# Kernel optimization log

Measured on AMD Instinct MI355X. Metric: run time of the kernel, lower is better.

The kernel has to match this reference:

```python
import jax, jax.numpy as jnp
import numpy as np

D = 256   # input_size
H = 512   # hidden_size
A = 4     # alpha_dim
K = 2 * A * A  # output values per input dim (binary=False -> 2 params)


def _masks():
    # MADE sequential-ordering masks, per DART.create_masks
    in_deg = np.arange(D)
    hid_deg = np.arange(H) % (D - 1)
    out_deg = np.arange(D) - 1  # arange(D) % D - 1
    m0 = (hid_deg[:, None] >= in_deg[None, :]).astype(np.float32)   # [H, D]
    mh = (hid_deg[:, None] >= hid_deg[None, :]).astype(np.float32)  # [H, H]
    ml = (out_deg[:, None] >= hid_deg[None, :]).astype(np.float32)  # [D, H]
    # repeat(1, K).view(-1, H): each output-dim row repeated K consecutive times
    ml = np.repeat(ml, K, axis=0)                                    # [D*K, H]
    return jnp.asarray(m0), jnp.asarray(mh), jnp.asarray(ml)


def setup_inputs() -> dict:
    key = jax.random.key(0)
    ks = jax.random.split(key, 10)
    B = 1024
    x = jax.random.normal(ks[0], (B, D), dtype=jnp.float32)
    def lin(k, out_dim, in_dim):
        s = 1.0 / np.sqrt(in_dim)
        kw, kb = jax.random.split(k)
        W = jax.random.uniform(kw, (out_dim, in_dim), jnp.float32, -s, s)
        b = jax.random.uniform(kb, (out_dim,), jnp.float32, -s, s)
        return W, b
    W0, b0 = lin(ks[1], H, D)
    W1, b1 = lin(ks[2], H, H)
    W2, b2 = lin(ks[3], H, H)
    Wout, bout = lin(ks[4], D * K, H)
    # unnormalized_log_p_alpha initialized to log(1/A)
    ulpa = jnp.full((1, D - 1, 1, A), -np.log(A), dtype=jnp.float32)
    return {"x": x, "W0": W0, "b0": b0, "W1": W1, "b1": b1,
            "W2": W2, "b2": b2, "Wout": Wout, "bout": bout, "ulpa": ulpa}


def reference(x, W0, b0, W1, b1, W2, b2, Wout, bout, ulpa):
    m0, mh, ml = _masks()
    B = x.shape[0]
    # masked MLP (MADE)
    h = jax.nn.relu(x @ (m0 * W0).T + b0)
    h = jax.nn.relu(h @ (mh * W1).T + b1)
    h = jax.nn.relu(h @ (mh * W2).T + b2)
    theta = (h @ (ml * Wout).T + bout).reshape(B, D, 2, A, A)
    mu = theta[:, :, 0]                      # [B, D, A, A]
    std = jnp.exp(theta[:, :, 1]) + 0.01     # [B, D, A, A]
    xe = x[:, :, None, None]
    # Normal log-prob
    log_px = -0.5 * jnp.square((xe - mu) / std) - jnp.log(std) - 0.5 * jnp.log(2.0 * jnp.pi)
    # normalized log p(alpha): [1, D-1, 1, A]
    lpa = jax.nn.log_softmax(ulpa, axis=-1)
    joint = log_px[:, :-1] + lpa             # [B, D-1, A, A]
    first = joint[:, 0, 0:1]                 # [B, 1, A]
    inner = jnp.swapaxes(joint[:, 1:], 0, 1)  # [D-2, B, A, A]
    # HMM-style forward recursion: stable log-domain chain matmul via scan
    def step(carry, m):
        # carry: [B, 1, A]; m: [B, A, A]
        new = jax.nn.logsumexp(carry[:, :, :, None] + m[:, None, :, :], axis=-2)
        return new, None
    carry, _ = jax.lax.scan(step, first, inner)
    last = log_px[:, -1, :, 0:1]             # [B, A, 1]
    log_p = jax.nn.logsumexp(carry[:, :, :, None] + last[:, None, :, :], axis=-2)  # [B,1,1]
    return log_p, theta
```

## Files before the change

### kernel.cpp

```cpp
#include <hip/hip_runtime.h>
#include <math.h>

#define Bsz 1024
#define Dd  256
#define Hh  512
#define NOUT 8192
#define C0f 0.91893853320467274178f

typedef __attribute__((ext_vector_type(8))) short bf8_t;
typedef __attribute__((ext_vector_type(4))) float f4_t;

__device__ inline ushort f2b(float f) {
  union { float f; unsigned u; } c; c.f = f;
  unsigned r = c.u + 0x7fffu + ((c.u >> 16) & 1u);
  return (ushort)(r >> 16);
}

__device__ inline void async16(const void* g, void* l) {
  __builtin_amdgcn_global_load_lds((const __attribute__((address_space(1))) void*)g,
                                   (__attribute__((address_space(3))) void*)l, 16, 0, 0);
}

__device__ inline int mod255(int v) {
  if (v >= 510) return v - 510;
  if (v >= 255) return v - 255;
  return v;
}

__global__ __launch_bounds__(256) void prep(
    const float* __restrict__ x,  const float* __restrict__ W0,
    const float* __restrict__ W1, const float* __restrict__ W2,
    const float* __restrict__ Wout, const float* __restrict__ ulpa,
    ushort* __restrict__ xb, ushort* __restrict__ w0b, ushort* __restrict__ w1b,
    ushort* __restrict__ w2b, ushort* __restrict__ woutb,
    float* __restrict__ lpa)
{
  const int blk = blockIdx.x, tid = threadIdx.x;
  if (blk == 2496) {
    if (tid < Dd - 1) {
      float v0 = ulpa[tid * 4 + 0], v1 = ulpa[tid * 4 + 1];
      float v2 = ulpa[tid * 4 + 2], v3 = ulpa[tid * 4 + 3];
      float m = fmaxf(fmaxf(v0, v1), fmaxf(v2, v3));
      float s = __expf(v0 - m) + __expf(v1 - m) + __expf(v2 - m) + __expf(v3 - m);
      float l = m + __logf(s);
      lpa[tid * 4 + 0] = v0 - l;
      lpa[tid * 4 + 1] = v1 - l;
      lpa[tid * 4 + 2] = v2 - l;
      lpa[tid * 4 + 3] = v3 - l;
    }
    return;
  }
  const float* src; ushort* dst; int lb, mode;
  if (blk < 128)      { src = x;    dst = xb;    lb = blk;       mode = 0; }
  else if (blk < 192) { src = W0;   dst = w0b;   lb = blk - 128; mode = 1; }
  else if (blk < 320) { src = W1;   dst = w1b;   lb = blk - 192; mode = 2; }
  else if (blk < 448) { src = W2;   dst = w2b;   lb = blk - 320; mode = 2; }
  else                { src = Wout; dst = woutb; lb = blk - 448; mode = 3; }

  const int e = lb * 2048 + tid * 8;
  float4 v0 = *(const float4*)(src + e);
  float4 v1 = *(const float4*)(src + e + 4);
  float vv[8] = {v0.x, v0.y, v0.z, v0.w, v1.x, v1.y, v1.z, v1.w};
  ushort u[8];
  if (mode == 0) {
#pragma unroll
    for (int i = 0; i < 8; i++) u[i] = f2b(vv[i]);
  } else if (mode == 1) {
    int n = e >> 8, k0 = e & 255, nd = mod255(n);
#pragma unroll
    for (int i = 0; i < 8; i++) u[i] = (nd >= k0 + i) ? f2b(vv[i]) : (ushort)0;
  } else if (mode == 2) {
    int n = e >> 9, k0 = e & 511, nd = mod255(n);
#pragma unroll
    for (int i = 0; i < 8; i++) u[i] = (nd >= mod255(k0 + i)) ? f2b(vv[i]) : (ushort)0;
  } else {
    int n = e >> 9, k0 = e & 511, nd = (n >> 5) - 1;
#pragma unroll
    for (int i = 0; i < 8; i++) u[i] = (nd >= mod255(k0 + i)) ? f2b(vv[i]) : (ushort)0;
  }
  *(ushort4*)(dst + e)     = *(ushort4*)&u[0];
  *(ushort4*)(dst + e + 4) = *(ushort4*)&u[4];
}

template<int KD>
__global__ __launch_bounds__(256) void gemm_s(
    const ushort* __restrict__ A, const ushort* __restrict__ W,
    const float* __restrict__ bias, ushort* __restrict__ Ch)
{
  __shared__ ushort As[64 * 64];
  __shared__ ushort Bs[32 * 64];
  const int tid = threadIdx.x, lane = tid & 63, wave = tid >> 6;
  const int row0 = blockIdx.y * 64, col0 = blockIdx.x * 32;
  const int fm = lane & 15, qq = lane >> 4;
  const int srow = lane >> 3, qslot = lane & 7;

  f4_t acc[2];
  acc[0] = (f4_t){0.f, 0.f, 0.f, 0.f};
  acc[1] = (f4_t){0.f, 0.f, 0.f, 0.f};

  for (int kt = 0; kt < KD; kt += 64) {
#pragma unroll
    for (int a = 0; a < 2; a++) {
      int rb = wave * 16 + a * 8;
      int r = rb + srow;
      int q = (qslot - r) & 7;
      async16(A + (size_t)(row0 + r) * KD + kt + q * 8, &As[rb * 64]);
    }
    {
      int rb = wave * 8;
      int r = rb + srow;
      int q = (qslot - r) & 7;
      async16(W + (size_t)(col0 + r) * KD + kt + q * 8, &Bs[rb * 64]);
    }
    __syncthreads();
#pragma unroll
    for (int t = 0; t < 2; t++) {
      int ra = wave * 16 + fm;
      int slota = ((t * 4 + qq) + ra) & 7;
      bf8_t af = *(const bf8_t*)&As[ra * 64 + slota * 8];
#pragma unroll
      for (int j = 0; j < 2; j++) {
        int rb = j * 16 + fm;
        int slot = ((t * 4 + qq) + rb) & 7;
        bf8_t bf = *(const bf8_t*)&Bs[rb * 64 + slot * 8];
        acc[j] = __builtin_amdgcn_mfma_f32_16x16x32_bf16(af, bf, acc[j], 0, 0, 0);
      }
    }
    __syncthreads();
  }

#pragma unroll
  for (int j = 0; j < 2; j++) {
    int col = col0 + j * 16 + fm;
    float bv = bias[col];
    int rbase = row0 + wave * 16 + qq * 4;
#pragma unroll
    for (int r = 0; r < 4; r++) {
      float t = fmaxf(acc[j][r] + bv, 0.0f);
      Ch[(size_t)(rbase + r) * Hh + col] = f2b(t);
    }
  }
}

__global__ __launch_bounds__(256) void gemm_big(
    const ushort* __restrict__ A, const ushort* __restrict__ W,
    const float* __restrict__ bias, float* __restrict__ Cf)
{
  __shared__ ushort As[128 * 64];
  __shared__ ushort Bs[64 * 64];
  const int tid = threadIdx.x, lane = tid & 63, wave = tid >> 6;
  const int waveM = wave >> 1, waveN = wave & 1;
  const int row0 = blockIdx.y * 128, col0 = blockIdx.x * 64;
  const int fm = lane & 15, qq = lane >> 4;
  const int srow = lane >> 3, qslot = lane & 7;
  const int Kd = Hh, N = NOUT;

  f4_t acc[4][2];
#pragma unroll
  for (int i = 0; i < 4; i++)
#pragma unroll
    for (int j = 0; j < 2; j++) acc[i][j] = (f4_t){0.f, 0.f, 0.f, 0.f};

  for (int kt = 0; kt < Kd; kt += 64) {
#pragma unroll
    for (int p = 0; p < 4; p++) {
      int rb = p * 32 + wave * 8;
      int r = rb + srow;
      int q = (qslot - r) & 7;
      async16(A + (size_t)(row0 + r) * Kd + kt + q * 8, &As[rb * 64]);
    }
#pragma unroll
    for (int p = 0; p < 2; p++) {
      int rb = p * 32 + wave * 8;
      int r = rb + srow;
      int q = (qslot - r) & 7;
      async16(W + (size_t)(col0 + r) * Kd + kt + q * 8, &Bs[rb * 64]);
    }
    __syncthreads();
#pragma unroll
    for (int t = 0; t < 2; t++) {
      bf8_t af[4], bf[2];
#pragma unroll
      for (int i = 0; i < 4; i++) {
        int r = waveM * 64 + i * 16 + fm;
        int slot = ((t * 4 + qq) + r) & 7;
        af[i] = *(const bf8_t*)&As[r * 64 + slot * 8];
      }
#pragma unroll
      for (int j = 0; j < 2; j++) {
        int r = waveN * 32 + j * 16 + fm;
        int slot = ((t * 4 + qq) + r) & 7;
        bf[j] = *(const bf8_t*)&Bs[r * 64 + slot * 8];
      }
#pragma unroll
      for (int i = 0; i < 4; i++)
#pragma unroll
        for (int j = 0; j < 2; j++)
          acc[i][j] = __builtin_amdgcn_mfma_f32_16x16x32_bf16(af[i], bf[j], acc[i][j], 0, 0, 0);
    }
    __syncthreads();
  }

#pragma unroll
  for (int j = 0; j < 2; j++) {
    int col = col0 + waveN * 32 + j * 16 + fm;
    float bv = bias[col];
#pragma unroll
    for (int i = 0; i < 4; i++) {
      int rbase = row0 + waveM * 64 + i * 16 + qq * 4;
#pragma unroll
      for (int r = 0; r < 4; r++)
        Cf[(size_t)(rbase + r) * N + col] = acc[i][j][r] + bv;
    }
  }
}

__global__ __launch_bounds__(256) void chain2(
    const float* __restrict__ x, const float* __restrict__ theta,
    const float* __restrict__ lpa, float* __restrict__ logp)
{
  __shared__ float ThS[NOUT];
  __shared__ float XS[Dd];
  __shared__ float Ts[16][16];
  const int b = blockIdx.x;
  const int tid = threadIdx.x, lane = tid & 63, wave = tid >> 6;
  const int seg = tid >> 4, e = tid & 15;
  const int i = e >> 2, jj = e & 3;
  const int base = lane & ~15;
  const float* th = theta + (size_t)b * NOUT;
  const float* xg = x + (size_t)b * Dd;

#pragma unroll
  for (int t = 0; t < 8; t++) {
    int off = (t * 4 + wave) * 256;
    async16(th + off + lane * 4, &ThS[off]);
  }
  if (wave == 0) async16(xg + lane * 4, &XS[0]);
  __syncthreads();

  const int d0 = 1 + seg * 16;
  const int d1 = min(d0 + 16, Dd - 1);

  auto stepm = [&](int d) -> float {
    float mu = ThS[d * 32 + e];
    float ls = ThS[d * 32 + 16 + e];
    float s  = __expf(ls) + 0.01f;
    float z  = (XS[d] - mu) * __builtin_amdgcn_rcpf(s);
    return -0.5f * z * z - __logf(s) - C0f + lpa[d * 4 + jj];
  };

  float T = stepm(d0);
  for (int d = d0 + 1; d < d1; d++) {
    float m_ = stepm(d);
    float v0 = __shfl(T, base + i * 4 + 0) + __shfl(m_, base + 0 * 4 + jj);
    float v1 = __shfl(T, base + i * 4 + 1) + __shfl(m_, base + 1 * 4 + jj);
    float v2 = __shfl(T, base + i * 4 + 2) + __shfl(m_, base + 2 * 4 + jj);
    float v3 = __shfl(T, base + i * 4 + 3) + __shfl(m_, base + 3 * 4 + jj);
    float mx = fmaxf(fmaxf(v0, v1), fmaxf(v2, v3));
    float s  = __expf(v0 - mx) + __expf(v1 - mx) + __expf(v2 - mx) + __expf(v3 - mx);
    T = mx + __logf(s);
  }
  Ts[seg][e] = T;
  __syncthreads();

  if (tid < 4) {
    const int j = tid;
    float mu = ThS[j], ls = ThS[16 + j];
    float s = __expf(ls) + 0.01f;
    float z = (XS[0] - mu) * __builtin_amdgcn_rcpf(s);
    float carry = -0.5f * z * z - __logf(s) - C0f + lpa[j];
#pragma unroll 1
    for (int sg = 0; sg < 16; sg++) {
      float c0 = __shfl(carry, 0);
      float c1 = __shfl(carry, 1);
      float c2 = __shfl(carry, 2);
      float c3 = __shfl(carry, 3);
      float v0 = c0 + Ts[sg][0 * 4 + j];
      float v1 = c1 + Ts[sg][1 * 4 + j];
      float v2 = c2 + Ts[sg][2 * 4 + j];
      float v3 = c3 + Ts[sg][3 * 4 + j];
      float mx = fmaxf(fmaxf(v0, v1), fmaxf(v2, v3));
      float ss = __expf(v0 - mx) + __expf(v1 - mx) + __expf(v2 - mx) + __expf(v3 - mx);
      carry = mx + __logf(ss);
    }
    float mu2 = ThS[255 * 32 + j * 4], ls2 = ThS[255 * 32 + 16 + j * 4];
    float s2 = __expf(ls2) + 0.01f;
    float z2 = (XS[255] - mu2) * __builtin_amdgcn_rcpf(s2);
    float v = carry - 0.5f * z2 * z2 - __logf(s2) - C0f;
    float mx = fmaxf(v, __shfl_xor(v, 1));
    mx = fmaxf(mx, __shfl_xor(mx, 2));
    float ee = __expf(v - mx);
    ee += __shfl_xor(ee, 1);
    ee += __shfl_xor(ee, 2);
    if (j == 0) logp[b] = mx + __logf(ee);
  }
}

extern "C" void kernel_launch(void* const* d_in, const int* in_sizes, int n_in,
                              void* d_out, int out_size, void* d_ws, size_t ws_size,
                              hipStream_t stream)
{
  const float* x    = (const float*)d_in[0];
  const float* W0   = (const float*)d_in[1];
  const float* b0   = (const float*)d_in[2];
  const float* W1   = (const float*)d_in[3];
  const float* b1   = (const float*)d_in[4];
  const float* W2   = (const float*)d_in[5];
  const float* b2   = (const float*)d_in[6];
  const float* Wout = (const float*)d_in[7];
  const float* bout = (const float*)d_in[8];
  const float* ulpa = (const float*)d_in[9];

  float* out   = (float*)d_out;
  float* logp  = out;
  float* theta = out + Bsz;

  ushort* ws    = (ushort*)d_ws;
  ushort* xb    = ws;
  ushort* w0b   = xb + 262144;
  ushort* w1b   = w0b + 131072;
  ushort* w2b   = w1b + 262144;
  ushort* woutb = w2b + 262144;
  ushort* h0    = woutb + 4194304;
  ushort* h1    = h0 + 524288;
  ushort* h2    = h1 + 524288;
  float*  lpa   = (float*)(h2 + 524288);

  prep<<<2497, 256, 0, stream>>>(x, W0, W1, W2, Wout, ulpa,
                                 xb, w0b, w1b, w2b, woutb, lpa);
  gemm_s<Dd><<<dim3(16, 16), 256, 0, stream>>>(xb, w0b, b0, h0);
  gemm_s<Hh><<<dim3(16, 16), 256, 0, stream>>>(h0, w1b, b1, h1);
  gemm_s<Hh><<<dim3(16, 16), 256, 0, stream>>>(h1, w2b, b2, h2);
  gemm_big<<<dim3(NOUT / 64, Bsz / 128), 256, 0, stream>>>(h2, woutb, bout, theta);
  chain2<<<Bsz, 256, 0, stream>>>(x, theta, lpa, logp);
}
```

Baseline: 139.0 us.

## Skip masked-zero K tiles in output GEMM and shrink hidden GEMM tiles

The output GEMM now skips K-tiles whose masked weights are all zero, based on the MADE mask structure for each column block. This cuts loads and MFMAs in the largest GEMM. The hidden-layer GEMMs move from 64x32 to 32x32 tiles with one MFMA accumulator per wave, doubling the number of blocks to improve occupancy on the small grids. The skip condition is hand-derived from the mask pattern and would silently give wrong results if the derivation is off.

```diff
diff --git a/kernel.cpp b/kernel.cpp
--- a/kernel.cpp
+++ b/kernel.cpp
@@ -87,58 +87,45 @@
     const ushort* __restrict__ A, const ushort* __restrict__ W,
     const float* __restrict__ bias, ushort* __restrict__ Ch)
 {
-  __shared__ ushort As[64 * 64];
+  __shared__ ushort As[32 * 64];
   __shared__ ushort Bs[32 * 64];
   const int tid = threadIdx.x, lane = tid & 63, wave = tid >> 6;
-  const int row0 = blockIdx.y * 64, col0 = blockIdx.x * 32;
+  const int row0 = blockIdx.y * 32, col0 = blockIdx.x * 32;
+  const int wi = wave >> 1, wj = wave & 1;
   const int fm = lane & 15, qq = lane >> 4;
   const int srow = lane >> 3, qslot = lane & 7;
 
-  f4_t acc[2];
-  acc[0] = (f4_t){0.f, 0.f, 0.f, 0.f};
-  acc[1] = (f4_t){0.f, 0.f, 0.f, 0.f};
+  f4_t acc = (f4_t){0.f, 0.f, 0.f, 0.f};
 
   for (int kt = 0; kt < KD; kt += 64) {
-#pragma unroll
-    for (int a = 0; a < 2; a++) {
-      int rb = wave * 16 + a * 8;
-      int r = rb + srow;
-      int q = (qslot - r) & 7;
-      async16(A + (size_t)(row0 + r) * KD + kt + q * 8, &As[rb * 64]);
-    }
     {
       int rb = wave * 8;
       int r = rb + srow;
       int q = (qslot - r) & 7;
+      async16(A + (size_t)(row0 + r) * KD + kt + q * 8, &As[rb * 64]);
       async16(W + (size_t)(col0 + r) * KD + kt + q * 8, &Bs[rb * 64]);
     }
     __syncthreads();
 #pragma unroll
     for (int t = 0; t < 2; t++) {
-      int ra = wave * 16 + fm;
+      int ra = wi * 16 + fm;
       int slota = ((t * 4 + qq) + ra) & 7;
       bf8_t af = *(const bf8_t*)&As[ra * 64 + slota * 8];
-#pragma unroll
-      for (int j = 0; j < 2; j++) {
-        int rb = j * 16 + fm;
-        int slot = ((t * 4 + qq) + rb) & 7;
-        bf8_t bf = *(const bf8_t*)&Bs[rb * 64 + slot * 8];
-        acc[j] = __builtin_amdgcn_mfma_f32_16x16x32_bf16(af, bf, acc[j], 0, 0, 0);
-      }
+      int rb = wj * 16 + fm;
+      int slot = ((t * 4 + qq) + rb) & 7;
+      bf8_t bf = *(const bf8_t*)&Bs[rb * 64 + slot * 8];
+      acc = __builtin_amdgcn_mfma_f32_16x16x32_bf16(af, bf, acc, 0, 0, 0);
     }
     __syncthreads();
   }
 
-#pragma unroll
-  for (int j = 0; j < 2; j++) {
-    int col = col0 + j * 16 + fm;
-    float bv = bias[col];
-    int rbase = row0 + wave * 16 + qq * 4;
-#pragma unroll
-    for (int r = 0; r < 4; r++) {
-      float t = fmaxf(acc[j][r] + bv, 0.0f);
-      Ch[(size_t)(rbase + r) * Hh + col] = f2b(t);
-    }
+  int col = col0 + wj * 16 + fm;
+  float bv = bias[col];
+  int rbase = row0 + wi * 16 + qq * 4;
+#pragma unroll
+  for (int r = 0; r < 4; r++) {
+    float t = fmaxf(acc[r] + bv, 0.0f);
+    Ch[(size_t)(rbase + r) * Hh + col] = f2b(t);
   }
 }
 
@@ -151,6 +138,7 @@
   const int tid = threadIdx.x, lane = tid & 63, wave = tid >> 6;
   const int waveM = wave >> 1, waveN = wave & 1;
   const int row0 = blockIdx.y * 128, col0 = blockIdx.x * 64;
+  const int dm = 2 * (int)blockIdx.x;
   const int fm = lane & 15, qq = lane >> 4;
   const int srow = lane >> 3, qslot = lane & 7;
   const int Kd = Hh, N = NOUT;
@@ -162,6 +150,8 @@
     for (int j = 0; j < 2; j++) acc[i][j] = (f4_t){0.f, 0.f, 0.f, 0.f};
 
   for (int kt = 0; kt < Kd; kt += 64) {
+    bool needed = (kt <= dm) || (kt >= 192 && kt <= 255 + dm) || (kt == 448);
+    if (!needed) continue;
 #pragma unroll
     for (int p = 0; p < 4; p++) {
       int rb = p * 32 + wave * 8;
@@ -328,9 +318,9 @@
 
   prep<<<2497, 256, 0, stream>>>(x, W0, W1, W2, Wout, ulpa,
                                  xb, w0b, w1b, w2b, woutb, lpa);
-  gemm_s<Dd><<<dim3(16, 16), 256, 0, stream>>>(xb, w0b, b0, h0);
-  gemm_s<Hh><<<dim3(16, 16), 256, 0, stream>>>(h0, w1b, b1, h1);
-  gemm_s<Hh><<<dim3(16, 16), 256, 0, stream>>>(h1, w2b, b2, h2);
+  gemm_s<Dd><<<dim3(16, 32), 256, 0, stream>>>(xb, w0b, b0, h0);
+  gemm_s<Hh><<<dim3(16, 32), 256, 0, stream>>>(h0, w1b, b1, h1);
+  gemm_s<Hh><<<dim3(16, 32), 256, 0, stream>>>(h1, w2b, b2, h2);
   gemm_big<<<dim3(NOUT / 64, Bsz / 128), 256, 0, stream>>>(h2, woutb, bout, theta);
   chain2<<<Bsz, 256, 0, stream>>>(x, theta, lpa, logp);
 }
```

New measurement: 138.6 us, median of 2. Within noise of the previous version (-0.3%).
